# Kernel tuning notes

Hardware: AMD Instinct MI355X
Metric: run time of the kernel (lower is better)

The kernel has to match this reference:

```python
import jax, jax.numpy as jnp
import numpy as np

N, S, E = 8, 1024, 768
H = 12
D = E // H  # head_dim = 64
FF = 4 * E
EPS = 1e-5


def setup_inputs() -> dict:
    key = jax.random.key(0)
    ks = jax.random.split(key, 12)
    s = lambda fan_in: 1.0 / np.sqrt(fan_in)
    return {
        "x": jax.random.normal(ks[0], (N, S, E), dtype=jnp.float32),
        "ln1_g": jnp.ones((E,), jnp.float32),
        "ln1_b": jnp.zeros((E,), jnp.float32),
        "ln2_g": jnp.ones((E,), jnp.float32),
        "ln2_b": jnp.zeros((E,), jnp.float32),
        "w_attn": jax.random.normal(ks[1], (E, 3 * E), jnp.float32) * s(E),
        "b_attn": jax.random.normal(ks[2], (3 * E,), jnp.float32) * 0.02,
        "w_proj": jax.random.normal(ks[3], (E, E), jnp.float32) * s(E),
        "b_proj": jax.random.normal(ks[4], (E,), jnp.float32) * 0.02,
        "w_fc": jax.random.normal(ks[5], (E, FF), jnp.float32) * s(E),
        "b_fc": jax.random.normal(ks[6], (FF,), jnp.float32) * 0.02,
        "w_fc2": jax.random.normal(ks[7], (FF, E), jnp.float32) * s(FF),
        "b_fc2": jax.random.normal(ks[8], (E,), jnp.float32) * 0.02,
    }


def _layernorm(x, g, b):
    mu = jnp.mean(x, axis=-1, keepdims=True)
    var = jnp.var(x, axis=-1, keepdims=True)
    return (x - mu) * jax.lax.rsqrt(var + EPS) * g + b


def reference(x, ln1_g, ln1_b, ln2_g, ln2_b, w_attn, b_attn, w_proj, b_proj,
              w_fc, b_fc, w_fc2, b_fc2):
    # --- attention branch (pre-LN) ---
    h = _layernorm(x, ln1_g, ln1_b)
    qkv = h @ w_attn + b_attn                       # [N,S,3E]
    q, k, v = jnp.split(qkv, 3, axis=-1)
    q = q.reshape(N, S, H, D).transpose(0, 2, 1, 3)  # [N,H,S,D]
    k = k.reshape(N, S, H, D).transpose(0, 2, 1, 3)
    v = v.reshape(N, S, H, D).transpose(0, 2, 1, 3)
    attn = jnp.einsum('nhsd,nhtd->nhst', q, k) * (1.0 / np.sqrt(D))
    causal = jnp.tril(jnp.ones((S, S), bool))
    attn = jnp.where(causal, attn, -jnp.inf)
    p = jax.nn.softmax(attn, axis=-1)
    out = jnp.einsum('nhst,nhtd->nhsd', p, v)        # [N,H,S,D]
    out = out.transpose(0, 2, 1, 3).reshape(N, S, E)
    x = x + (out @ w_proj + b_proj)
    # --- MLP branch ---
    h2 = _layernorm(x, ln2_g, ln2_b)
    ff = jax.nn.gelu(h2 @ w_fc + b_fc, approximate=False)  # exact GELU (torch nn.GELU default)
    x = x + (ff @ w_fc2 + b_fc2)
    return x
```

## Files before the change

### kernel.cpp

```cpp
#include <hip/hip_runtime.h>
#include <hip/hip_bf16.h>
#include <stdint.h>

#define S_LEN 1024
#define E_DIM 768
#define H_N   12
#define FF_DIM 3072

typedef __hip_bfloat16 bf16;
using short8  = __attribute__((ext_vector_type(8))) short;
using short4v = __attribute__((ext_vector_type(4))) short;
using f32x4   = __attribute__((ext_vector_type(4))) float;

__device__ __forceinline__ void async_cp16(const void* g, void* l) {
  __builtin_amdgcn_global_load_lds(
      (__attribute__((address_space(1))) void*)(g),
      (__attribute__((address_space(3))) void*)(l), 16, 0, 0);
}

__global__ __launch_bounds__(256) void wcastT_all(
    const float* __restrict__ wa, const float* __restrict__ wp,
    const float* __restrict__ wf, const float* __restrict__ wf2,
    bf16* __restrict__ oa, bf16* __restrict__ op,
    bf16* __restrict__ of, bf16* __restrict__ of2) {
  __shared__ float t[32][33];
  int bid = blockIdx.x;
  const float* w; bf16* wt; int K, N, bx, by;
  if (bid < 1728)      { w = wa;  wt = oa;  K = 768;  N = 2304; int r = bid;        bx = r % 72; by = r / 72; }
  else if (bid < 2304) { w = wp;  wt = op;  K = 768;  N = 768;  int r = bid - 1728; bx = r % 24; by = r / 24; }
  else if (bid < 4608) { w = wf;  wt = of;  K = 768;  N = 3072; int r = bid - 2304; bx = r % 96; by = r / 96; }
  else                 { w = wf2; wt = of2; K = 3072; N = 768;  int r = bid - 4608; bx = r % 24; by = r / 24; }
  int x = threadIdx.x & 31;
  int y = threadIdx.x >> 5;
  for (int i = y; i < 32; i += 8)
    t[i][x] = w[(size_t)(by * 32 + i) * N + bx * 32 + x];
  __syncthreads();
  for (int i = y; i < 32; i += 8)
    wt[(size_t)(bx * 32 + i) * K + by * 32 + x] = __float2bfloat16(t[x][i]);
}

__global__ __launch_bounds__(256) void ln_rows(const float* __restrict__ x,
                                               const float* __restrict__ g,
                                               const float* __restrict__ b,
                                               bf16* __restrict__ out) {
  int row = blockIdx.x;
  int tid = threadIdx.x;
  const float* xr = x + (size_t)row * E_DIM;
  float v0 = xr[tid], v1 = xr[tid + 256], v2 = xr[tid + 512];
  float s = v0 + v1 + v2;
  float ss = v0 * v0 + v1 * v1 + v2 * v2;
  for (int o = 32; o > 0; o >>= 1) {
    s  += __shfl_down(s, o);
    ss += __shfl_down(ss, o);
  }
  __shared__ float ps[4], pq[4];
  int wv = tid >> 6;
  if ((tid & 63) == 0) { ps[wv] = s; pq[wv] = ss; }
  __syncthreads();
  s  = ps[0] + ps[1] + ps[2] + ps[3];
  ss = pq[0] + pq[1] + pq[2] + pq[3];
  float mu  = s * (1.0f / E_DIM);
  float var = ss * (1.0f / E_DIM) - mu * mu;
  float rs  = rsqrtf(var + 1e-5f);
  bf16* orow = out + (size_t)row * E_DIM;
  orow[tid]       = __float2bfloat16((v0 - mu) * rs * g[tid]       + b[tid]);
  orow[tid + 256] = __float2bfloat16((v1 - mu) * rs * g[tid + 256] + b[tid + 256]);
  orow[tid + 512] = __float2bfloat16((v2 - mu) * rs * g[tid + 512] + b[tid + 512]);
}

__global__ __launch_bounds__(256) void scatter_v(const bf16* __restrict__ qkv,
                                                 bf16* __restrict__ vtb) {
  int blk = blockIdx.x;
  int n = blk >> 7, soct = blk & 127;
  int tid = threadIdx.x;
  for (int j = tid; j < 768; j += 256) {
    int h = j >> 6, d = j & 63;
    const bf16* src = qkv + ((size_t)(n * 1024 + soct * 8)) * 2304 + 1536 + h * 64 + d;
    short8 v;
#pragma unroll
    for (int i = 0; i < 8; i++)
      v[i] = __builtin_bit_cast(short, src[(size_t)i * 2304]);
    *(short8*)&vtb[((((size_t)n * 12 + h) * 128 + soct) * 64 + d) * 8] = v;
  }
}

template <int MODE>
__global__ __launch_bounds__(512, 2) void gemm8(
    const bf16* __restrict__ A, const bf16* __restrict__ Bt,
    const float* __restrict__ bias, bf16* __restrict__ outb,
    int M, int N, int K) {
  __shared__ __align__(16) bf16 smem[49152];
  bf16 (*lA)[16384] = reinterpret_cast<bf16(*)[16384]>(smem);
  bf16 (*lB)[8192]  = reinterpret_cast<bf16(*)[8192]>(smem + 32768);
  int tid = threadIdx.x;
  int w = tid >> 6, lane = tid & 63;
  int quad = lane >> 4, l16 = lane & 15;
  int wr = w >> 2, wc = w & 3;
  int gx = N >> 7;
  int flat = blockIdx.x;
  int y8 = flat & 7;
  int q2 = flat >> 3;
  int bx = q2 % gx;
  int by = (q2 / gx) * 8 + y8;
  int m0 = by << 8, n0 = bx << 7;

  f32x4 acc[8][2];
#pragma unroll
  for (int i = 0; i < 8; i++)
#pragma unroll
    for (int j = 0; j < 2; j++)
#pragma unroll
      for (int r = 0; r < 4; r++) acc[i][j][r] = 0.f;

  int xs = l16 & 7;
  int ko0 = (quad ^ xs) << 3;
  int ko1 = ((4 + quad) ^ xs) << 3;
  int sgo = ((tid & 7) ^ ((tid >> 3) & 7)) << 3;
  size_t aRB = (size_t)(m0 + (tid >> 3)) * K + sgo;
  size_t bRB = (size_t)(n0 + (tid >> 3)) * K + sgo;
  int aD = tid * 8;
  int bD = tid * 8;

  auto stA = [&](int buf, int mh, int kt) {
#pragma unroll
    for (int p = 0; p < 2; ++p)
      async_cp16(A + aRB + (size_t)(p * 128 + mh * 64) * K + (size_t)kt * 64,
                 &lA[buf][aD + mh * 4096 + p * 8192]);
  };
  auto stB = [&](int buf, int kt) {
#pragma unroll
    for (int p = 0; p < 2; ++p)
      async_cp16(Bt + bRB + (size_t)(p * 64) * K + (size_t)kt * 64,
                 &lB[buf][bD + p * 4096]);
  };

  short8 af[4][2], bf[2][2];

#define LD_A(BUF, MH)                                                        \
  {                                                                          \
    _Pragma("unroll") for (int i = 0; i < 4; ++i) {                          \
      const bf16* bp =                                                       \
          &lA[BUF][(MH)*4096 + wr * 8192 + (i * 16 + l16) * 64];             \
      af[i][0] = *(const short8*)&bp[ko0];                                   \
      af[i][1] = *(const short8*)&bp[ko1];                                   \
    }                                                                        \
  }
#define LD_B(BUF)                                                            \
  {                                                                          \
    _Pragma("unroll") for (int j = 0; j < 2; ++j) {                          \
      int rb = wc * 32 + j * 16 + l16;                                       \
      const bf16* bp = &lB[BUF][((rb >> 6) << 12) + ((rb & 63) << 6)];       \
      bf[j][0] = *(const short8*)&bp[ko0];                                   \
      bf[j][1] = *(const short8*)&bp[ko1];                                   \
    }                                                                        \
  }
#define DO_MFMA(MH)                                                          \
  {                                                                          \
    __builtin_amdgcn_s_setprio(1);                                           \
    _Pragma("unroll") for (int ks = 0; ks < 2; ++ks)                         \
        _Pragma("unroll") for (int i = 0; i < 4; ++i)                        \
            _Pragma("unroll") for (int j = 0; j < 2; ++j)                    \
                acc[(MH)*4 + i][j] =                                         \
        __builtin_amdgcn_mfma_f32_16x16x32_bf16(                             \
            bf[j][ks], af[i][ks], acc[(MH)*4 + i][j], 0, 0, 0);              \
    __builtin_amdgcn_s_setprio(0);                                           \
  }
#define BAR() __builtin_amdgcn_s_barrier()
#define LGKM0() asm volatile("s_waitcnt lgkmcnt(0)" ::: "memory")
#define VM4() asm volatile("s_waitcnt vmcnt(4)" ::: "memory")
#define VM0() asm volatile("s_waitcnt vmcnt(0)" ::: "memory")

  stA(0, 0, 0); stA(0, 1, 0); stB(0, 0);
  stA(1, 0, 1); stB(1, 1);
  VM4();
  BAR();

  int nit = K >> 7;
  for (int it = 0; it < nit; ++it) {
    int ktA = 2 * it + 2, ktB = 2 * it + 3;
    bool more = (it + 1 < nit);
    LD_A(0, 0); LD_B(0);
    stA(1, 1, 2 * it + 1);
    BAR(); LGKM0(); DO_MFMA(0); BAR();
    LD_A(0, 1);
    if (more) { stA(0, 0, ktA); stB(0, ktA); VM4(); } else { VM0(); }
    BAR(); LGKM0(); DO_MFMA(1); BAR();
    LD_A(1, 0); LD_B(1);
    if (more) stA(0, 1, ktA);
    BAR(); LGKM0(); DO_MFMA(0); BAR();
    LD_A(1, 1);
    if (more) { stA(1, 0, ktB); stB(1, ktB); VM4(); }
    BAR(); LGKM0(); DO_MFMA(1); BAR();
  }

  {
    bf16* wbuf = smem + w * 5120;
#pragma unroll
    for (int nj = 0; nj < 2; ++nj) {
      int lc = nj * 16 + quad * 4;
      int colb = n0 + wc * 32 + lc;
      f32x4 b4 = *(const f32x4*)&bias[colb];
      float sc = (MODE == 1 && colb < 768) ? 0.125f : 1.0f;
#pragma unroll
      for (int mi = 0; mi < 8; ++mi) {
        f32x4 v = acc[mi][nj] + b4;
        short4v pk;
        if (MODE == 1) {
          for (int r = 0; r < 4; r++)
            pk[r] = __builtin_bit_cast(short, __float2bfloat16(v[r] * sc));
        } else {
          for (int r = 0; r < 4; r++) {
            float x = v[r];
            float t = x * (1.59576912161f + 0.0713548162726f * x * x);
            float g = x * __builtin_amdgcn_rcpf(1.0f + __expf(-t));
            pk[r] = __builtin_bit_cast(short, __float2bfloat16(g));
          }
        }
        *(short4v*)&wbuf[(mi * 16 + l16) * 40 + lc] = pk;
      }
    }
    asm volatile("s_waitcnt lgkmcnt(0)" ::: "memory");
#pragma unroll
    for (int p = 0; p < 8; ++p) {
      int chunk = p * 64 + lane;
      int r = chunk >> 2, c8 = (chunk & 3) * 8;
      short8 vv = *(const short8*)&wbuf[r * 40 + c8];
      *(short8*)&outb[(size_t)(m0 + wr * 128 + r) * N + n0 + wc * 32 + c8] = vv;
    }
  }
#undef LD_A
#undef LD_B
#undef DO_MFMA
#undef BAR
#undef LGKM0
#undef VM4
#undef VM0
}

__global__ __launch_bounds__(256) void gemm_bt64(
    const bf16* __restrict__ A, const bf16* __restrict__ Bt,
    const float* __restrict__ bias, const float* __restrict__ resid,
    float* __restrict__ outf, int M, int N, int K) {
  __shared__ bf16 As[2][128 * 64];
  __shared__ bf16 Bs[2][64 * 64];
  int tid = threadIdx.x;
  int wave = tid >> 6, lane = tid & 63;
  int quad = lane >> 4, l16 = lane & 15;
  int gx = N >> 6;
  int flat = blockIdx.x;
  int y8 = flat & 7;
  int q2 = flat >> 3;
  int bx = q2 % gx;
  int by = (q2 / gx) * 8 + y8;
  int m0 = by * 128, n0 = bx * 64;
  int wm = wave * 32;
  f32x4 acc[2][4];
  for (int i = 0; i < 2; i++)
    for (int j = 0; j < 4; j++)
      for (int r = 0; r < 4; r++) acc[i][j][r] = 0.f;

  int xs = l16 & 7;
  int srow = tid >> 3;
  int scg = (((tid & 7) ^ (srow & 7)) << 3);
  const bf16* aptr = A  + (size_t)(m0 + srow) * K + scg;
  const bf16* bptr = Bt + (size_t)(n0 + srow) * K + scg;
  int ldst = tid * 8;

#pragma unroll
  for (int t = 0; t < 4; t++)
    async_cp16(aptr + (size_t)t * 32 * K, &As[0][ldst + t * 2048]);
#pragma unroll
  for (int t = 0; t < 2; t++)
    async_cp16(bptr + (size_t)t * 32 * K, &Bs[0][ldst + t * 2048]);

  int nkb = K >> 6;
  for (int ik = 0; ik < nkb; ++ik) {
    int cur = ik & 1;
    if (ik + 1 < nkb) {
      size_t ko = (size_t)(ik + 1) * 64;
#pragma unroll
      for (int t = 0; t < 4; t++)
        async_cp16(aptr + ko + (size_t)t * 32 * K, &As[cur ^ 1][ldst + t * 2048]);
#pragma unroll
      for (int t = 0; t < 2; t++)
        async_cp16(bptr + ko + (size_t)t * 32 * K, &Bs[cur ^ 1][ldst + t * 2048]);
      asm volatile("s_waitcnt vmcnt(6)" ::: "memory");
    } else {
      asm volatile("s_waitcnt vmcnt(0)" ::: "memory");
    }
    __builtin_amdgcn_s_barrier();
    asm volatile("" ::: "memory");
#pragma unroll
    for (int ks = 0; ks < 2; ks++) {
      int ko2 = (((ks * 4 + quad) ^ xs) << 3);
      short8 af[2], bfr[4];
      for (int i = 0; i < 2; i++)
        af[i] = *(const short8*)&As[cur][(wm + i * 16 + l16) * 64 + ko2];
      for (int j = 0; j < 4; j++)
        bfr[j] = *(const short8*)&Bs[cur][(j * 16 + l16) * 64 + ko2];
      for (int i = 0; i < 2; i++)
        for (int j = 0; j < 4; j++)
          acc[i][j] = __builtin_amdgcn_mfma_f32_16x16x32_bf16(
              bfr[j], af[i], acc[i][j], 0, 0, 0);
    }
    asm volatile("" ::: "memory");
    __builtin_amdgcn_s_barrier();
  }

  for (int j = 0; j < 4; j++) {
    int colb = n0 + j * 16 + quad * 4;
    f32x4 b4 = *(const f32x4*)&bias[colb];
    for (int i = 0; i < 2; i++) {
      int row = m0 + wm + i * 16 + l16;
      size_t idx = (size_t)row * N + colb;
      f32x4 rv = *(const f32x4*)&resid[idx];
      *(f32x4*)&outf[idx] = acc[i][j] + b4 + rv;
    }
  }
}

__global__ __launch_bounds__(256) void attn_fwd(
    const bf16* __restrict__ qkv, const bf16* __restrict__ vg,
    bf16* __restrict__ out) {
  __shared__ bf16 kt2[2][8 * 64 * 8];
  __shared__ bf16 vt2[2][8 * 64 * 8];
  __shared__ bf16 pba[4][16 * 68];
  __shared__ bf16 pbb[4][16 * 68];
  int flat = blockIdx.x;
  int xcd = flat & 7;
  int j = flat >> 3;
  int a = j & 7;
  int g = j >> 3;
  int nh = xcd * 12 + g;
  int b = 15 - a;
  int n = nh / H_N, h = nh % H_N;
  int tid = threadIdx.x, wave = tid >> 6, lane = tid & 63;
  int quad = lane >> 4, l16 = lane & 15;
  const bf16* qp = qkv + (size_t)n * S_LEN * 2304 + (size_t)h * 64;
  const bf16* vp = vg + (size_t)nh * 128 * 64 * 8;
  int qra = a * 64 + wave * 16;
  int qrb = b * 64 + wave * 16;

  short8 qfa[2], qfb[2];
  qfa[0] = *(const short8*)&qp[(size_t)(qra + l16) * 2304 + quad * 8];
  qfa[1] = *(const short8*)&qp[(size_t)(qra + l16) * 2304 + 32 + quad * 8];
  qfb[0] = *(const short8*)&qp[(size_t)(qrb + l16) * 2304 + quad * 8];
  qfb[1] = *(const short8*)&qp[(size_t)(qrb + l16) * 2304 + 32 + quad * 8];

  const bf16* kbase = qkv + ((size_t)n * S_LEN + (tid & 63)) * 2304 + 768 +
                      h * 64 + ((tid >> 6) << 3);
  const bf16* vbase = vp + (((size_t)(tid >> 6) * 64) + (tid & 63)) * 8;

  f32x4 oaa[4], oab[4];
  for (int dt = 0; dt < 4; dt++)
    for (int r = 0; r < 4; r++) { oaa[dt][r] = 0.f; oab[dt][r] = 0.f; }
  float lia = 0.f, lib = 0.f;

  {
    bf16* lk = &kt2[0][0] + tid * 8;
    bf16* lv = &vt2[0][0] + tid * 8;
#pragma unroll
    for (int t = 0; t < 2; ++t) {
      async_cp16(kbase + t * 32, lk + t * 2048);
      async_cp16(vbase + (size_t)t * 2048, lv + t * 2048);
    }
  }

  for (int kb = 0; kb <= b; ++kb) {
    bool act_a = (kb <= a);
    int cur = kb & 1;
    __syncthreads();

    short8 kf[2][4], vf[2][4];
#pragma unroll
    for (int ks = 0; ks < 2; ks++)
      for (int nt = 0; nt < 4; nt++) {
        kf[ks][nt] = *(const short8*)
            &kt2[cur][(size_t)((ks * 4 + quad) * 64 + nt * 16 + l16) * 8];
        vf[ks][nt] = *(const short8*)
            &vt2[cur][(size_t)((ks * 4 + quad) * 64 + nt * 16 + l16) * 8];
      }
    if (kb < b) {
      bf16* lk = &kt2[cur ^ 1][0] + tid * 8;
      bf16* lv = &vt2[cur ^ 1][0] + tid * 8;
      size_t kko = (size_t)(kb + 1) * 64 * 2304;
      size_t vko = (size_t)(kb + 1) * 4096;
#pragma unroll
      for (int t = 0; t < 2; ++t) {
        async_cp16(kbase + kko + t * 32, lk + t * 2048);
        async_cp16(vbase + vko + (size_t)t * 2048, lv + t * 2048);
      }
    }

    f32x4 sb4[4], sa4[4];
    for (int nt = 0; nt < 4; nt++) {
      for (int r = 0; r < 4; r++) { sb4[nt][r] = -10.f; sa4[nt][r] = -10.f; }
      for (int ks = 0; ks < 2; ks++) {
        sb4[nt] = __builtin_amdgcn_mfma_f32_16x16x32_bf16(kf[ks][nt], qfb[ks],
                                                          sb4[nt], 0, 0, 0);
        if (act_a)
          sa4[nt] = __builtin_amdgcn_mfma_f32_16x16x32_bf16(kf[ks][nt], qfa[ks],
                                                            sa4[nt], 0, 0, 0);
      }
    }
    if (kb == b) {
      int ql = wave * 16 + l16;
      for (int nt = 0; nt < 4; nt++)
        for (int r = 0; r < 4; r++)
          if (nt * 16 + quad * 4 + r > ql) sb4[nt][r] = -INFINITY;
    }
    if (kb == a) {
      int ql = wave * 16 + l16;
      for (int nt = 0; nt < 4; nt++)
        for (int r = 0; r < 4; r++)
          if (nt * 16 + quad * 4 + r > ql) sa4[nt][r] = -INFINITY;
    }

    float rsb = 0.f;
    for (int nt = 0; nt < 4; nt++)
      for (int r = 0; r < 4; r++) {
        float p = __expf(sb4[nt][r]);
        sb4[nt][r] = p;
        rsb += p;
      }
    rsb += __shfl_xor(rsb, 16);
    rsb += __shfl_xor(rsb, 32);
    lib += rsb;
    bf16* pwb = pbb[wave];
    for (int nt = 0; nt < 4; nt++) {
      short4v pk;
      for (int r = 0; r < 4; r++)
        pk[r] = __builtin_bit_cast(short, __float2bfloat16(sb4[nt][r]));
      *(short4v*)&pwb[l16 * 68 + nt * 16 + quad * 4] = pk;
    }
    if (act_a) {
      float rsa = 0.f;
      for (int nt = 0; nt < 4; nt++)
        for (int r = 0; r < 4; r++) {
          float p = __expf(sa4[nt][r]);
          sa4[nt][r] = p;
          rsa += p;
        }
      rsa += __shfl_xor(rsa, 16);
      rsa += __shfl_xor(rsa, 32);
      lia += rsa;
      bf16* pwa = pba[wave];
      for (int nt = 0; nt < 4; nt++) {
        short4v pk;
        for (int r = 0; r < 4; r++)
          pk[r] = __builtin_bit_cast(short, __float2bfloat16(sa4[nt][r]));
        *(short4v*)&pwa[l16 * 68 + nt * 16 + quad * 4] = pk;
      }
    }
    asm volatile("s_waitcnt lgkmcnt(0)" ::: "memory");

    for (int ks = 0; ks < 2; ks++) {
      short8 pfb = *(const short8*)&pbb[wave][l16 * 68 + ks * 32 + quad * 8];
      short8 pfa;
      if (act_a) pfa = *(const short8*)&pba[wave][l16 * 68 + ks * 32 + quad * 8];
      for (int dt = 0; dt < 4; dt++) {
        oab[dt] = __builtin_amdgcn_mfma_f32_16x16x32_bf16(vf[ks][dt], pfb,
                                                          oab[dt], 0, 0, 0);
        if (act_a)
          oaa[dt] = __builtin_amdgcn_mfma_f32_16x16x32_bf16(vf[ks][dt], pfa,
                                                            oaa[dt], 0, 0, 0);
      }
    }
  }

  float inva = 1.0f / lia, invb = 1.0f / lib;
  int ta = n * S_LEN + qra + l16;
  int tb = n * S_LEN + qrb + l16;
  for (int dt = 0; dt < 4; dt++) {
    short4v ova, ovb;
    for (int r = 0; r < 4; r++) {
      ova[r] = __builtin_bit_cast(short, __float2bfloat16(oaa[dt][r] * inva));
      ovb[r] = __builtin_bit_cast(short, __float2bfloat16(oab[dt][r] * invb));
    }
    *(short4v*)&out[(size_t)ta * E_DIM + h * 64 + dt * 16 + quad * 4] = ova;
    *(short4v*)&out[(size_t)tb * E_DIM + h * 64 + dt * 16 + quad * 4] = ovb;
  }
}

extern "C" void kernel_launch(void* const* d_in, const int* in_sizes, int n_in,
                              void* d_out, int out_size, void* d_ws, size_t ws_size,
                              hipStream_t stream) {
  (void)in_sizes; (void)n_in; (void)out_size; (void)ws_size;
  const float* x      = (const float*)d_in[0];
  const float* ln1_g  = (const float*)d_in[1];
  const float* ln1_b  = (const float*)d_in[2];
  const float* ln2_g  = (const float*)d_in[3];
  const float* ln2_b  = (const float*)d_in[4];
  const float* w_attn = (const float*)d_in[5];
  const float* b_attn = (const float*)d_in[6];
  const float* w_proj = (const float*)d_in[7];
  const float* b_proj = (const float*)d_in[8];
  const float* w_fc   = (const float*)d_in[9];
  const float* b_fc   = (const float*)d_in[10];
  const float* w_fc2  = (const float*)d_in[11];
  const float* b_fc2  = (const float*)d_in[12];
  float* out = (float*)d_out;

  char* ws = (char*)d_ws;
  bf16* wt_attn = (bf16*)(ws);
  bf16* wt_proj = (bf16*)(ws + 3538944);
  bf16* wt_fc   = (bf16*)(ws + 4718592);
  bf16* wt_fc2  = (bf16*)(ws + 9437184);
  bf16* hbuf    = (bf16*)(ws + 14155776);
  float* x2     = (float*)(ws + 26738688);
  bf16* qkvb    = (bf16*)(ws + 51904512);
  bf16* vtb     = (bf16*)(ws + 89653248);
  bf16* ao      = hbuf;
  bf16* ff      = qkvb;

  dim3 blk(256);
  wcastT_all<<<dim3(6912), blk, 0, stream>>>(w_attn, w_proj, w_fc, w_fc2,
                                             wt_attn, wt_proj, wt_fc, wt_fc2);

  ln_rows<<<8192, blk, 0, stream>>>(x, ln1_g, ln1_b, hbuf);

  gemm8<1><<<dim3(576), dim3(512), 0, stream>>>(
      hbuf, wt_attn, b_attn, qkvb, 8192, 2304, 768);

  scatter_v<<<dim3(1024), blk, 0, stream>>>(qkvb, vtb);

  attn_fwd<<<dim3(768), blk, 0, stream>>>(qkvb, vtb, ao);

  gemm_bt64<<<dim3(12 * 64), blk, 0, stream>>>(
      ao, wt_proj, b_proj, x, x2, 8192, 768, 768);

  ln_rows<<<8192, blk, 0, stream>>>(x2, ln2_g, ln2_b, hbuf);

  gemm8<2><<<dim3(768), dim3(512), 0, stream>>>(
      hbuf, wt_fc, b_fc, ff, 8192, 3072, 768);

  gemm_bt64<<<dim3(12 * 64), blk, 0, stream>>>(
      ff, wt_fc2, b_fc2, x2, out, 8192, 768, 3072);
}
```

Measured before the change: 345.2 us.

## Triple-buffer LDS in gemm8 with full-tile prefetch two k-steps ahead

Reworks the gemm8 main loop from a double-buffered, half-tile-staggered schedule to a three-buffer ring. Each k-tile of A and B is prefetched two steps ahead and waited on with vmcnt(6). This gives global loads more time in flight before the MFMA work needs them. LDS grows from 96KB to 144KB, so launch bounds drop to one block per CU, trading occupancy for deeper prefetch. The unrolled-by-3 loop assumes K/64 is a multiple of 3, which holds for K=768 and 3072.

```diff
diff --git a/kernel.cpp b/kernel.cpp
--- a/kernel.cpp
+++ b/kernel.cpp
@@ -85,13 +85,11 @@
 }
 
 template <int MODE>
-__global__ __launch_bounds__(512, 2) void gemm8(
+__global__ __launch_bounds__(512, 1) void gemm8(
     const bf16* __restrict__ A, const bf16* __restrict__ Bt,
     const float* __restrict__ bias, bf16* __restrict__ outb,
     int M, int N, int K) {
-  __shared__ __align__(16) bf16 smem[49152];
-  bf16 (*lA)[16384] = reinterpret_cast<bf16(*)[16384]>(smem);
-  bf16 (*lB)[8192]  = reinterpret_cast<bf16(*)[8192]>(smem + 32768);
+  __shared__ __align__(16) bf16 smem[73728];
   int tid = threadIdx.x;
   int w = tid >> 6, lane = tid & 63;
   int quad = lane >> 4, l16 = lane & 15;
@@ -125,13 +123,13 @@
 #pragma unroll
     for (int p = 0; p < 2; ++p)
       async_cp16(A + aRB + (size_t)(p * 128 + mh * 64) * K + (size_t)kt * 64,
-                 &lA[buf][aD + mh * 4096 + p * 8192]);
+                 &smem[buf * 24576 + aD + mh * 4096 + p * 8192]);
   };
   auto stB = [&](int buf, int kt) {
 #pragma unroll
     for (int p = 0; p < 2; ++p)
       async_cp16(Bt + bRB + (size_t)(p * 64) * K + (size_t)kt * 64,
-                 &lB[buf][bD + p * 4096]);
+                 &smem[buf * 24576 + 16384 + bD + p * 4096]);
   };
 
   short8 af[4][2], bf[2][2];
@@ -140,7 +138,7 @@
   {                                                                          \
     _Pragma("unroll") for (int i = 0; i < 4; ++i) {                          \
       const bf16* bp =                                                       \
-          &lA[BUF][(MH)*4096 + wr * 8192 + (i * 16 + l16) * 64];             \
+          &smem[(BUF)*24576 + (MH)*4096 + wr * 8192 + (i * 16 + l16) * 64];  \
       af[i][0] = *(const short8*)&bp[ko0];                                   \
       af[i][1] = *(const short8*)&bp[ko1];                                   \
     }                                                                        \
@@ -149,7 +147,8 @@
   {                                                                          \
     _Pragma("unroll") for (int j = 0; j < 2; ++j) {                          \
       int rb = wc * 32 + j * 16 + l16;                                       \
-      const bf16* bp = &lB[BUF][((rb >> 6) << 12) + ((rb & 63) << 6)];       \
+      const bf16* bp =                                                       \
+          &smem[(BUF)*24576 + 16384 + ((rb >> 6) << 12) + ((rb & 63) << 6)]; \
       bf[j][0] = *(const short8*)&bp[ko0];                                   \
       bf[j][1] = *(const short8*)&bp[ko1];                                   \
     }                                                                        \
@@ -167,30 +166,31 @@
   }
 #define BAR() __builtin_amdgcn_s_barrier()
 #define LGKM0() asm volatile("s_waitcnt lgkmcnt(0)" ::: "memory")
-#define VM4() asm volatile("s_waitcnt vmcnt(4)" ::: "memory")
+#define VM6() asm volatile("s_waitcnt vmcnt(6)" ::: "memory")
 #define VM0() asm volatile("s_waitcnt vmcnt(0)" ::: "memory")
 
+  int nkt = K >> 6;
+
   stA(0, 0, 0); stA(0, 1, 0); stB(0, 0);
-  stA(1, 0, 1); stB(1, 1);
-  VM4();
+  stA(1, 0, 1); stA(1, 1, 1); stB(1, 1);
+  VM6();
   BAR();
 
-  int nit = K >> 7;
-  for (int it = 0; it < nit; ++it) {
-    int ktA = 2 * it + 2, ktB = 2 * it + 3;
-    bool more = (it + 1 < nit);
-    LD_A(0, 0); LD_B(0);
-    stA(1, 1, 2 * it + 1);
-    BAR(); LGKM0(); DO_MFMA(0); BAR();
-    LD_A(0, 1);
-    if (more) { stA(0, 0, ktA); stB(0, ktA); VM4(); } else { VM0(); }
-    BAR(); LGKM0(); DO_MFMA(1); BAR();
-    LD_A(1, 0); LD_B(1);
-    if (more) stA(0, 1, ktA);
-    BAR(); LGKM0(); DO_MFMA(0); BAR();
-    LD_A(1, 1);
-    if (more) { stA(1, 0, ktB); stB(1, ktB); VM4(); }
-    BAR(); LGKM0(); DO_MFMA(1); BAR();
+#define STEP(B, NB, T)                                                       \
+  {                                                                          \
+    LD_A(B, 0); LD_B(B);                                                     \
+    if ((T) + 2 < nkt) { stA(NB, 0, (T) + 2); stB(NB, (T) + 2); }            \
+    BAR(); LGKM0(); DO_MFMA(0); BAR();                                       \
+    LD_A(B, 1);                                                              \
+    if ((T) + 2 < nkt) { stA(NB, 1, (T) + 2); VM6(); }                       \
+    else if ((T) + 1 < nkt) { VM0(); }                                       \
+    BAR(); LGKM0(); DO_MFMA(1); BAR();                                       \
+  }
+
+  for (int t3 = 0; t3 < nkt; t3 += 3) {
+    STEP(0, 2, t3);
+    STEP(1, 0, t3 + 1);
+    STEP(2, 1, t3 + 2);
   }
 
   {
@@ -233,8 +233,9 @@
 #undef DO_MFMA
 #undef BAR
 #undef LGKM0
-#undef VM4
+#undef VM6
 #undef VM0
+#undef STEP
 }
 
 __global__ __launch_bounds__(256) void gemm_bt64(
```

After: 368.5 us. 1.07x slower.

## Pre-pack K into fragment layout and load attention K/V straight from global

Applied to the files above, without the earlier changes.

Extends the V scatter kernel to also repack K per head into a fragment-friendly contiguous layout stored in the x2 workspace region, which is unused at that point. The attention kernel drops its double-buffered LDS staging, async copies and per-iteration barrier, and reads K and V MFMA fragments directly from global memory. This removes LDS traffic and block-wide syncs, but it relies on L2/cache for reuse across waves and gives up the explicit prefetch overlap. It also adds an extra K write and read pass.

```diff
diff --git a/kernel.cpp b/kernel.cpp
--- a/kernel.cpp
+++ b/kernel.cpp
@@ -68,11 +68,19 @@
   orow[tid + 512] = __float2bfloat16((v2 - mu) * rs * g[tid + 512] + b[tid + 512]);
 }
 
-__global__ __launch_bounds__(256) void scatter_v(const bf16* __restrict__ qkv,
-                                                 bf16* __restrict__ vtb) {
+__global__ __launch_bounds__(256) void scatter_kv(const bf16* __restrict__ qkv,
+                                                  bf16* __restrict__ kbuf,
+                                                  bf16* __restrict__ vtb) {
   int blk = blockIdx.x;
   int n = blk >> 7, soct = blk & 127;
   int tid = threadIdx.x;
+  for (int j = tid; j < 768; j += 256) {
+    int h = j >> 6, r = j & 63, c = r >> 3, i = r & 7;
+    int s = soct * 8 + i;
+    short8 v = *(const short8*)&qkv[((size_t)(n * 1024 + s)) * 2304 + 768 +
+                                    h * 64 + c * 8];
+    *(short8*)&kbuf[((((size_t)n * 12 + h) * 8 + c) * 1024 + s) * 8] = v;
+  }
   for (int j = tid; j < 768; j += 256) {
     int h = j >> 6, d = j & 63;
     const bf16* src = qkv + ((size_t)(n * 1024 + soct * 8)) * 2304 + 1536 + h * 64 + d;
@@ -320,10 +328,8 @@
 }
 
 __global__ __launch_bounds__(256) void attn_fwd(
-    const bf16* __restrict__ qkv, const bf16* __restrict__ vg,
-    bf16* __restrict__ out) {
-  __shared__ bf16 kt2[2][8 * 64 * 8];
-  __shared__ bf16 vt2[2][8 * 64 * 8];
+    const bf16* __restrict__ qkv, const bf16* __restrict__ kg,
+    const bf16* __restrict__ vg, bf16* __restrict__ out) {
   __shared__ bf16 pba[4][16 * 68];
   __shared__ bf16 pbb[4][16 * 68];
   int flat = blockIdx.x;
@@ -337,6 +343,7 @@
   int tid = threadIdx.x, wave = tid >> 6, lane = tid & 63;
   int quad = lane >> 4, l16 = lane & 15;
   const bf16* qp = qkv + (size_t)n * S_LEN * 2304 + (size_t)h * 64;
+  const bf16* kp = kg + (size_t)nh * 8 * S_LEN * 8;
   const bf16* vp = vg + (size_t)nh * 128 * 64 * 8;
   int qra = a * 64 + wave * 16;
   int qrb = b * 64 + wave * 16;
@@ -347,50 +354,25 @@
   qfb[0] = *(const short8*)&qp[(size_t)(qrb + l16) * 2304 + quad * 8];
   qfb[1] = *(const short8*)&qp[(size_t)(qrb + l16) * 2304 + 32 + quad * 8];
 
-  const bf16* kbase = qkv + ((size_t)n * S_LEN + (tid & 63)) * 2304 + 768 +
-                      h * 64 + ((tid >> 6) << 3);
-  const bf16* vbase = vp + (((size_t)(tid >> 6) * 64) + (tid & 63)) * 8;
-
   f32x4 oaa[4], oab[4];
   for (int dt = 0; dt < 4; dt++)
     for (int r = 0; r < 4; r++) { oaa[dt][r] = 0.f; oab[dt][r] = 0.f; }
   float lia = 0.f, lib = 0.f;
 
-  {
-    bf16* lk = &kt2[0][0] + tid * 8;
-    bf16* lv = &vt2[0][0] + tid * 8;
-#pragma unroll
-    for (int t = 0; t < 2; ++t) {
-      async_cp16(kbase + t * 32, lk + t * 2048);
-      async_cp16(vbase + (size_t)t * 2048, lv + t * 2048);
-    }
-  }
-
   for (int kb = 0; kb <= b; ++kb) {
     bool act_a = (kb <= a);
-    int cur = kb & 1;
-    __syncthreads();
 
     short8 kf[2][4], vf[2][4];
 #pragma unroll
     for (int ks = 0; ks < 2; ks++)
+#pragma unroll
       for (int nt = 0; nt < 4; nt++) {
         kf[ks][nt] = *(const short8*)
-            &kt2[cur][(size_t)((ks * 4 + quad) * 64 + nt * 16 + l16) * 8];
+            &kp[((size_t)(ks * 4 + quad) * S_LEN + kb * 64 + nt * 16 + l16) * 8];
         vf[ks][nt] = *(const short8*)
-            &vt2[cur][(size_t)((ks * 4 + quad) * 64 + nt * 16 + l16) * 8];
+            &vp[(size_t)kb * 4096 +
+                (size_t)((ks * 4 + quad) * 64 + nt * 16 + l16) * 8];
       }
-    if (kb < b) {
-      bf16* lk = &kt2[cur ^ 1][0] + tid * 8;
-      bf16* lv = &vt2[cur ^ 1][0] + tid * 8;
-      size_t kko = (size_t)(kb + 1) * 64 * 2304;
-      size_t vko = (size_t)(kb + 1) * 4096;
-#pragma unroll
-      for (int t = 0; t < 2; ++t) {
-        async_cp16(kbase + kko + t * 32, lk + t * 2048);
-        async_cp16(vbase + vko + (size_t)t * 2048, lv + t * 2048);
-      }
-    }
 
     f32x4 sb4[4], sa4[4];
     for (int nt = 0; nt < 4; nt++) {
@@ -510,6 +492,7 @@
   float* x2     = (float*)(ws + 26738688);
   bf16* qkvb    = (bf16*)(ws + 51904512);
   bf16* vtb     = (bf16*)(ws + 89653248);
+  bf16* kbuf    = (bf16*)(ws + 26738688);
   bf16* ao      = hbuf;
   bf16* ff      = qkvb;
 
@@ -522,9 +505,9 @@
   gemm8<1><<<dim3(576), dim3(512), 0, stream>>>(
       hbuf, wt_attn, b_attn, qkvb, 8192, 2304, 768);
 
-  scatter_v<<<dim3(1024), blk, 0, stream>>>(qkvb, vtb);
-
-  attn_fwd<<<dim3(768), blk, 0, stream>>>(qkvb, vtb, ao);
+  scatter_kv<<<dim3(1024), blk, 0, stream>>>(qkvb, kbuf, vtb);
+
+  attn_fwd<<<dim3(768), blk, 0, stream>>>(qkvb, kbuf, vtb, ao);
 
   gemm_bt64<<<dim3(12 * 64), blk, 0, stream>>>(
       ao, wt_proj, b_proj, x, x2, 8192, 768, 768);
```

Result: slower. 395.1 us (+14.5%).
